# Kernel tuning notes

Hardware: AMD Instinct MI355X
Metric: run time of the kernel (lower is better)

## Reference

```python
import jax, jax.numpy as jnp
import numpy as np

N_SAMPLES = 8192
N_EDGES = 4096
INPUT_DIM = 512
DK = 64
OUTPUT_DIM = 256


def setup_inputs() -> dict:
    key = jax.random.key(0)
    k1, k2, k3, k4, k5, k6 = jax.random.split(key, 6)

    def xavier(k, shape):
        bound = np.sqrt(6.0 / (shape[0] + shape[1])).astype(np.float32)
        return jax.random.uniform(k, shape, jnp.float32, -bound, bound)

    X = jax.random.normal(k1, (N_SAMPLES, INPUT_DIM), jnp.float32)
    Y = jax.random.normal(k2, (N_EDGES, INPUT_DIM), jnp.float32)
    H = jax.random.randint(k3, (N_SAMPLES, N_EDGES), 0, 2, jnp.int32)
    W_q = xavier(k4, (INPUT_DIM, DK))
    W_k = xavier(k5, (INPUT_DIM, DK))
    W_v = xavier(k6, (INPUT_DIM, OUTPUT_DIM))
    return {"X": X, "Y": Y, "H": H, "W_q": W_q, "W_k": W_k, "W_v": W_v}


def reference(X, Y, H, W_q, W_k, W_v):
    # Q: (n_edges, dk), K: (n_samples, dk)
    Q = Y @ W_q
    K = X @ W_k
    scale = jnp.sqrt(jnp.asarray(K.shape[1], jnp.float32))
    # scores: (n_edges, n_samples), masked by hypergraph incidence H.T
    scores = (Q @ K.T) / scale
    scores = jnp.where(H.T == 0, -jnp.inf, scores)
    attn = jax.nn.softmax(scores, axis=-1)
    # attention-weighted vertex features projected by W_v
    return attn @ (X @ W_v)
```

## Files before the change

kernel.cpp:

```cpp
#include <hip/hip_runtime.h>
#include <hip/hip_bf16.h>

#define NS 8192
#define NE 4096
#define DIN 512
#define DK 64
#define DV 256
#define NCHUNK 8
#define CHUNK (NS / NCHUNK)
#define NTILE (CHUNK / 64)

typedef __attribute__((ext_vector_type(8))) short bf16x8;
typedef __attribute__((ext_vector_type(4))) float f32x4;
typedef __attribute__((ext_vector_type(8))) unsigned short ushort8;
typedef __attribute__((ext_vector_type(4))) unsigned short ushort4v;

#define L2E 1.44269504088896f

__device__ __forceinline__ unsigned short f2bf(float f) {
    union { float f; unsigned int u; } v; v.f = f;
    unsigned int u = v.u;
    unsigned int r = u + 0x7fffu + ((u >> 16) & 1u);
    return (unsigned short)(r >> 16);
}

union ProjSmem {
    struct { unsigned short As[64][40]; unsigned short Bst[64][40]; } s;
    unsigned short Ct[64][72];
};

__global__ __launch_bounds__(256, 4) void proj_kernel(
    const float* __restrict__ X, const float* __restrict__ Y,
    const float* __restrict__ Wq, const float* __restrict__ Wk,
    const float* __restrict__ Wv, const int* __restrict__ H,
    unsigned short* __restrict__ Qb, unsigned short* __restrict__ Kb,
    unsigned short* __restrict__ Vt, unsigned int* __restrict__ Hb) {

    int b = blockIdx.x;
    int tid = threadIdx.x;

    if (b >= 704) {
        int pb = b - 704;
        int sg = pb >> 4;
        int e  = (pb & 15) * 256 + tid;
        unsigned word = 0;
        #pragma unroll
        for (int k = 0; k < 32; ++k)
            word |= (unsigned)(H[(size_t)(sg * 32 + k) * NE + e] & 1) << k;
        Hb[(size_t)sg * NE + e] = word;
        return;
    }

    const float* A; const float* B; unsigned short* out;
    int N, m0, n0; float scale; bool tr;
    if (b < 64)       { A = Y; B = Wq; out = Qb; N = 64;  m0 = b * 64;        n0 = 0;            scale = 0.125f * L2E; tr = false; }
    else if (b < 192) { A = X; B = Wk; out = Kb; N = 64;  m0 = (b - 64) * 64; n0 = 0;            scale = 1.0f;         tr = false; }
    else              { int bb = b - 192;
                        A = X; B = Wv; out = Vt; N = 256; m0 = (bb >> 2) * 64; n0 = (bb & 3) * 64; scale = 1.0f;       tr = true; }

    __shared__ ProjSmem sm;
    int lane = tid & 63, w = tid >> 6;
    int c = lane & 15, g = lane >> 4;
    int wr = w >> 1, wc = w & 1;

    f32x4 acc[2][2] = {};

    for (int kt = 0; kt < 16; ++kt) {
        int k0 = kt * 32;
        __syncthreads();
        #pragma unroll
        for (int it = 0; it < 2; ++it) {
            int idx = it * 256 + tid;
            {
                int r = idx >> 3, c4 = (idx & 7) * 4;
                float4 v = *(const float4*)&A[(size_t)(m0 + r) * DIN + k0 + c4];
                ushort4v t; t.x = f2bf(v.x); t.y = f2bf(v.y); t.z = f2bf(v.z); t.w = f2bf(v.w);
                *(ushort4v*)&sm.s.As[r][c4] = t;
            }
            {
                int kk = idx >> 4, c4 = (idx & 15) * 4;
                float4 v = *(const float4*)&B[(size_t)(k0 + kk) * N + n0 + c4];
                sm.s.Bst[c4 + 0][kk] = f2bf(v.x);
                sm.s.Bst[c4 + 1][kk] = f2bf(v.y);
                sm.s.Bst[c4 + 2][kk] = f2bf(v.z);
                sm.s.Bst[c4 + 3][kk] = f2bf(v.w);
            }
        }
        __syncthreads();

        bf16x8 af[2], bfr[2];
        #pragma unroll
        for (int fr = 0; fr < 2; ++fr)
            af[fr] = *(const bf16x8*)&sm.s.As[wr * 32 + fr * 16 + c][8 * g];
        #pragma unroll
        for (int fc = 0; fc < 2; ++fc)
            bfr[fc] = *(const bf16x8*)&sm.s.Bst[wc * 32 + fc * 16 + c][8 * g];
        #pragma unroll
        for (int fr = 0; fr < 2; ++fr)
            #pragma unroll
            for (int fc = 0; fc < 2; ++fc)
                acc[fr][fc] = __builtin_amdgcn_mfma_f32_16x16x32_bf16(af[fr], bfr[fc], acc[fr][fc], 0, 0, 0);
    }

    if (!tr) {
        #pragma unroll
        for (int fr = 0; fr < 2; ++fr)
            #pragma unroll
            for (int fc = 0; fc < 2; ++fc)
                #pragma unroll
                for (int i = 0; i < 4; ++i) {
                    int row = wr * 32 + fr * 16 + 4 * g + i;
                    int col = wc * 32 + fc * 16 + c;
                    out[(size_t)(m0 + row) * N + n0 + col] = f2bf(acc[fr][fc][i] * scale);
                }
    } else {
        __syncthreads();
        #pragma unroll
        for (int fr = 0; fr < 2; ++fr)
            #pragma unroll
            for (int fc = 0; fc < 2; ++fc)
                #pragma unroll
                for (int i = 0; i < 4; ++i) {
                    int row = wr * 32 + fr * 16 + 4 * g + i;
                    int col = wc * 32 + fc * 16 + c;
                    sm.Ct[col][row] = f2bf(acc[fr][fc][i]);
                }
        __syncthreads();
        int nl = tid >> 2, q = tid & 3;
        #pragma unroll
        for (int gg = 0; gg < 2; ++gg) {
            int G = q * 2 + gg;
            int ks = G >> 2, gq = G & 3;
            union { ushort4v h[2]; ushort8 v8; } u;
            u.h[0] = *(const ushort4v*)&sm.Ct[nl][ks * 32 + gq * 4];
            u.h[1] = *(const ushort4v*)&sm.Ct[nl][ks * 32 + 16 + gq * 4];
            *(ushort8*)&out[(size_t)(n0 + nl) * NS + m0 + G * 8] = u.v8;
        }
    }
}

__global__ __launch_bounds__(256, 2) void flash_kernel(
    const unsigned short* __restrict__ Qb, const unsigned short* __restrict__ Kb,
    const unsigned short* __restrict__ Vt, const unsigned int* __restrict__ Hb,
    unsigned int* __restrict__ pacc, float* __restrict__ pm, float* __restrict__ pl) {

    int bid = blockIdx.x;
    int ch = bid & 7, eb = bid >> 3;
    int e0 = eb * 64;
    int sbeg = ch * CHUNK;

    __shared__ unsigned short smem[20480];

    int tid = threadIdx.x, lane = tid & 63, w = tid >> 6;
    int c = lane & 15, g = lane >> 4;
    int eW = e0 + w * 16 + c;
    int cc = tid & 7;
    int swz = (c & 7) << 3;

    bf16x8 qf[2];
    #pragma unroll
    for (int ks = 0; ks < 2; ++ks)
        qf[ks] = *(const bf16x8*)&Qb[(size_t)eW * DK + ks * 32 + 8 * g];

    const unsigned short* baseK[2];
    const unsigned short* baseV[2];
    #pragma unroll
    for (int ks = 0; ks < 2; ++ks) {
        baseK[ks] = &smem[(c * 64 + ks * 32 + 8 * g) ^ swz];
        baseV[ks] = &smem[4096 + ((c * 64 + ks * 32 + 8 * g) ^ swz)];
    }

    int r0 = tid >> 3;
    int cs = cc ^ (r0 & 7);
    const unsigned short* gK[2];
    const unsigned short* gV[8];
    #pragma unroll
    for (int it = 0; it < 2; ++it)
        gK[it] = &Kb[(size_t)(sbeg + it * 32 + r0) * DK + cs * 8];
    #pragma unroll
    for (int it = 0; it < 8; ++it)
        gV[it] = &Vt[(size_t)(it * 32 + r0) * NS + sbeg + cs * 8];

    const unsigned int* hb0 = &Hb[(size_t)(sbeg >> 5) * NE + eW];
    const unsigned int* hb1 = hb0 + NE;

    f32x4 o[16] = {};
    float m = -1e30f, l = 0.0f;

    #pragma unroll 1
    for (int t = 0; t < NTILE; ++t) {
        __syncthreads();

        unsigned hw0 = *hb0; unsigned hw1 = *hb1;
        hb0 += 2 * NE; hb1 += 2 * NE;

        #pragma unroll
        for (int it = 0; it < 2; ++it) {
            __builtin_amdgcn_global_load_lds(
                (const void*)gK[it],
                (void*)((char*)smem + (it * 256 + w * 64) * 16), 16, 0, 0);
            gK[it] += 64 * DK;
        }
        #pragma unroll
        for (int it = 0; it < 8; ++it) {
            __builtin_amdgcn_global_load_lds(
                (const void*)gV[it],
                (void*)((char*)smem + 8192 + (it * 256 + w * 64) * 16), 16, 0, 0);
            gV[it] += 64;
        }

        __syncthreads();

        __builtin_amdgcn_s_setprio(1);
        f32x4 st[4] = {};
        #pragma unroll
        for (int ks = 0; ks < 2; ++ks)
            #pragma unroll
            for (int fr = 0; fr < 4; ++fr) {
                bf16x8 a = *(const bf16x8*)&baseK[ks][fr * 1024];
                st[fr] = __builtin_amdgcn_mfma_f32_16x16x32_bf16(a, qf[ks], st[fr], 0, 0, 0);
            }
        __builtin_amdgcn_s_setprio(0);

        unsigned hs[2] = { hw0 >> (4 * g), hw1 >> (4 * g) };
        float pmax = -1e30f;
        #pragma unroll
        for (int fr = 0; fr < 4; ++fr) {
            unsigned hsf = hs[fr >> 1] >> ((fr & 1) * 16);
            #pragma unroll
            for (int i = 0; i < 4; ++i) {
                float sv = ((hsf >> i) & 1u) ? st[fr][i] : -1e30f;
                st[fr][i] = sv;
                pmax = fmaxf(pmax, sv);
            }
        }
        pmax = fmaxf(pmax, __shfl_xor(pmax, 16));
        pmax = fmaxf(pmax, __shfl_xor(pmax, 32));

        if (!__all(pmax <= m + 8.0f)) {
            float mn = fmaxf(m, pmax);
            float al = exp2f(m - mn);
            l *= al;
            #pragma unroll
            for (int vb = 0; vb < 16; ++vb) o[vb] *= al;
            m = mn;
        }

        float lp = 0.0f;
        #pragma unroll
        for (int fr = 0; fr < 4; ++fr)
            #pragma unroll
            for (int i = 0; i < 4; ++i) {
                float e = exp2f(st[fr][i] - m);
                st[fr][i] = e;
                lp += e;
            }
        lp += __shfl_xor(lp, 16);
        lp += __shfl_xor(lp, 32);
        l += lp;

        unsigned int pk[8];
        #pragma unroll
        for (int fr = 0; fr < 4; ++fr)
            #pragma unroll
            for (int hf = 0; hf < 2; ++hf) {
                union { __hip_bfloat162 h; unsigned int u; } cv;
                cv.h = __float22bfloat162_rn(make_float2(st[fr][2 * hf], st[fr][2 * hf + 1]));
                pk[fr * 2 + hf] = cv.u;
            }

        __builtin_amdgcn_s_setprio(1);
        #pragma unroll
        for (int ks = 0; ks < 2; ++ks) {
            union { unsigned int u[4]; bf16x8 s; } bb;
            bb.u[0] = pk[4 * ks]; bb.u[1] = pk[4 * ks + 1];
            bb.u[2] = pk[4 * ks + 2]; bb.u[3] = pk[4 * ks + 3];
            #pragma unroll
            for (int vb = 0; vb < 16; ++vb) {
                bf16x8 av = *(const bf16x8*)&baseV[ks][vb * 1024];
                o[vb] = __builtin_amdgcn_mfma_f32_16x16x32_bf16(av, bb.s, o[vb], 0, 0, 0);
            }
        }
        __builtin_amdgcn_s_setprio(0);
    }

    size_t base = (size_t)ch * (DV / 2) * NE;
    #pragma unroll
    for (int vb = 0; vb < 16; ++vb)
        #pragma unroll
        for (int ip = 0; ip < 2; ++ip) {
            union { __hip_bfloat162 h; unsigned int u; } cv;
            cv.h = __float22bfloat162_rn(make_float2(o[vb][2 * ip], o[vb][2 * ip + 1]));
            pacc[base + (size_t)(vb * 8 + 2 * g + ip) * NE + eW] = cv.u;
        }
    if (g == 0) {
        pm[ch * NE + eW] = m;
        pl[ch * NE + eW] = l;
    }
}

__global__ __launch_bounds__(256, 4) void combine_kernel(
    const unsigned int* __restrict__ pacc, const float* __restrict__ pm,
    const float* __restrict__ pl, float* __restrict__ out) {

    __shared__ float T[64][68];
    int bid = blockIdx.x;
    int eb = bid & 63, vb = bid >> 6;
    int e0 = eb * 64, v0 = vb * 64;
    int tid = threadIdx.x;
    int el = tid & 63, vh = tid >> 6;
    int e = e0 + el;

    float mv[NCHUNK]; float M = -1e30f;
    #pragma unroll
    for (int chn = 0; chn < NCHUNK; ++chn) {
        mv[chn] = pm[chn * NE + e];
        M = fmaxf(M, mv[chn]);
    }
    float den = 0.0f; float wch[NCHUNK];
    #pragma unroll
    for (int chn = 0; chn < NCHUNK; ++chn) {
        wch[chn] = exp2f(mv[chn] - M);
        den += wch[chn] * pl[chn * NE + e];
    }
    float rden = 1.0f / den;

    #pragma unroll
    for (int kp = 0; kp < 8; ++kp) {
        int vp = vb * 32 + vh * 8 + kp;
        float n0 = 0.0f, n1 = 0.0f;
        #pragma unroll
        for (int chn = 0; chn < NCHUNK; ++chn) {
            unsigned int pk = pacc[((size_t)chn * (DV / 2) + vp) * NE + e];
            n0 += wch[chn] * __uint_as_float(pk << 16);
            n1 += wch[chn] * __uint_as_float(pk & 0xffff0000u);
        }
        T[el][(vh * 8 + kp) * 2]     = n0 * rden;
        T[el][(vh * 8 + kp) * 2 + 1] = n1 * rden;
    }
    __syncthreads();

    int er = tid >> 2, c16 = (tid & 3) * 16;
    #pragma unroll
    for (int j = 0; j < 4; ++j) {
        float4 vv = *(const float4*)&T[er][c16 + 4 * j];
        *(float4*)&out[(size_t)(e0 + er) * DV + v0 + c16 + 4 * j] = vv;
    }
}

#define QB_OFF   ((size_t)0)
#define KB_OFF   (QB_OFF + (size_t)NE * DK * 2)
#define VT_OFF   (KB_OFF + (size_t)NS * DK * 2)
#define PACC_OFF (VT_OFF + (size_t)DV * NS * 2)
#define PM_OFF   (PACC_OFF + (size_t)NCHUNK * (DV / 2) * NE * 4)
#define PL_OFF   (PM_OFF + (size_t)NCHUNK * NE * 4)
#define HB_OFF   (PL_OFF + (size_t)NCHUNK * NE * 4)

extern "C" void kernel_launch(void* const* d_in, const int* in_sizes, int n_in,
                              void* d_out, int out_size, void* d_ws, size_t ws_size,
                              hipStream_t stream) {
    const float* X  = (const float*)d_in[0];
    const float* Y  = (const float*)d_in[1];
    const int*   H  = (const int*)d_in[2];
    const float* Wq = (const float*)d_in[3];
    const float* Wk = (const float*)d_in[4];
    const float* Wv = (const float*)d_in[5];

    char* ws = (char*)d_ws;
    unsigned short* Qb = (unsigned short*)(ws + QB_OFF);
    unsigned short* Kb = (unsigned short*)(ws + KB_OFF);
    unsigned short* Vt = (unsigned short*)(ws + VT_OFF);
    unsigned int* pacc = (unsigned int*)(ws + PACC_OFF);
    float* pm   = (float*)(ws + PM_OFF);
    float* pl   = (float*)(ws + PL_OFF);
    unsigned int* Hb = (unsigned int*)(ws + HB_OFF);

    proj_kernel<<<4800, 256, 0, stream>>>(X, Y, Wq, Wk, Wv, H, Qb, Kb, Vt, Hb);
    flash_kernel<<<512, 256, 0, stream>>>(Qb, Kb, Vt, Hb, pacc, pm, pl);
    combine_kernel<<<256, 256, 0, stream>>>(pacc, pm, pl, (float*)d_out);
}
```

Measured before the change: 92.70 us.

## Stream raw int32 mask tiles into LDS inside flash kernel, drop bit-packing pass

Removes the separate pass in the projection kernel that packed the int32 incidence matrix into bitmasks. The flash kernel now pulls 64x64 int32 mask tiles straight from global memory into LDS with async global_load_lds, alongside the K/V tiles, and reads each mask value from LDS. This saves one full read of H plus the bitmask write and read. In exchange the flash kernel moves 4x more mask bytes per tile through its loads, needs more LDS (which may lower occupancy), and adds LDS reads in the masking step.

```diff
diff --git a/kernel.cpp b/kernel.cpp
--- a/kernel.cpp
+++ b/kernel.cpp
@@ -32,24 +32,12 @@
 __global__ __launch_bounds__(256, 4) void proj_kernel(
     const float* __restrict__ X, const float* __restrict__ Y,
     const float* __restrict__ Wq, const float* __restrict__ Wk,
-    const float* __restrict__ Wv, const int* __restrict__ H,
+    const float* __restrict__ Wv,
     unsigned short* __restrict__ Qb, unsigned short* __restrict__ Kb,
-    unsigned short* __restrict__ Vt, unsigned int* __restrict__ Hb) {
+    unsigned short* __restrict__ Vt) {
 
     int b = blockIdx.x;
     int tid = threadIdx.x;
-
-    if (b >= 704) {
-        int pb = b - 704;
-        int sg = pb >> 4;
-        int e  = (pb & 15) * 256 + tid;
-        unsigned word = 0;
-        #pragma unroll
-        for (int k = 0; k < 32; ++k)
-            word |= (unsigned)(H[(size_t)(sg * 32 + k) * NE + e] & 1) << k;
-        Hb[(size_t)sg * NE + e] = word;
-        return;
-    }
 
     const float* A; const float* B; unsigned short* out;
     int N, m0, n0; float scale; bool tr;
@@ -141,7 +129,7 @@
 
 __global__ __launch_bounds__(256, 2) void flash_kernel(
     const unsigned short* __restrict__ Qb, const unsigned short* __restrict__ Kb,
-    const unsigned short* __restrict__ Vt, const unsigned int* __restrict__ Hb,
+    const unsigned short* __restrict__ Vt, const int* __restrict__ H,
     unsigned int* __restrict__ pacc, float* __restrict__ pm, float* __restrict__ pl) {
 
     int bid = blockIdx.x;
@@ -149,7 +137,7 @@
     int e0 = eb * 64;
     int sbeg = ch * CHUNK;
 
-    __shared__ unsigned short smem[20480];
+    __shared__ unsigned short smem[28672];
 
     int tid = threadIdx.x, lane = tid & 63, w = tid >> 6;
     int c = lane & 15, g = lane >> 4;
@@ -169,20 +157,22 @@
         baseK[ks] = &smem[(c * 64 + ks * 32 + 8 * g) ^ swz];
         baseV[ks] = &smem[4096 + ((c * 64 + ks * 32 + 8 * g) ^ swz)];
     }
+    const int* hL = (const int*)((const char*)smem + 40960) + g * 256 + w * 16 + c;
 
     int r0 = tid >> 3;
     int cs = cc ^ (r0 & 7);
     const unsigned short* gK[2];
     const unsigned short* gV[8];
+    const int* gH[4];
     #pragma unroll
     for (int it = 0; it < 2; ++it)
         gK[it] = &Kb[(size_t)(sbeg + it * 32 + r0) * DK + cs * 8];
     #pragma unroll
     for (int it = 0; it < 8; ++it)
         gV[it] = &Vt[(size_t)(it * 32 + r0) * NS + sbeg + cs * 8];
-
-    const unsigned int* hb0 = &Hb[(size_t)(sbeg >> 5) * NE + eW];
-    const unsigned int* hb1 = hb0 + NE;
+    #pragma unroll
+    for (int it = 0; it < 4; ++it)
+        gH[it] = &H[(size_t)(sbeg + it * 16 + (tid >> 4)) * NE + e0 + (tid & 15) * 4];
 
     f32x4 o[16] = {};
     float m = -1e30f, l = 0.0f;
@@ -190,9 +180,6 @@
     #pragma unroll 1
     for (int t = 0; t < NTILE; ++t) {
         __syncthreads();
-
-        unsigned hw0 = *hb0; unsigned hw1 = *hb1;
-        hb0 += 2 * NE; hb1 += 2 * NE;
 
         #pragma unroll
         for (int it = 0; it < 2; ++it) {
@@ -208,6 +195,13 @@
                 (void*)((char*)smem + 8192 + (it * 256 + w * 64) * 16), 16, 0, 0);
             gV[it] += 64;
         }
+        #pragma unroll
+        for (int it = 0; it < 4; ++it) {
+            __builtin_amdgcn_global_load_lds(
+                (const void*)gH[it],
+                (void*)((char*)smem + 40960 + (it * 256 + w * 64) * 16), 16, 0, 0);
+            gH[it] += 64 * NE;
+        }
 
         __syncthreads();
 
@@ -222,18 +216,16 @@
             }
         __builtin_amdgcn_s_setprio(0);
 
-        unsigned hs[2] = { hw0 >> (4 * g), hw1 >> (4 * g) };
         float pmax = -1e30f;
         #pragma unroll
-        for (int fr = 0; fr < 4; ++fr) {
-            unsigned hsf = hs[fr >> 1] >> ((fr & 1) * 16);
+        for (int fr = 0; fr < 4; ++fr)
             #pragma unroll
             for (int i = 0; i < 4; ++i) {
-                float sv = ((hsf >> i) & 1u) ? st[fr][i] : -1e30f;
+                int hv = hL[fr * 1024 + i * 64];
+                float sv = hv ? st[fr][i] : -1e30f;
                 st[fr][i] = sv;
                 pmax = fmaxf(pmax, sv);
             }
-        }
         pmax = fmaxf(pmax, __shfl_xor(pmax, 16));
         pmax = fmaxf(pmax, __shfl_xor(pmax, 32));
 
@@ -354,7 +346,6 @@
 #define PACC_OFF (VT_OFF + (size_t)DV * NS * 2)
 #define PM_OFF   (PACC_OFF + (size_t)NCHUNK * (DV / 2) * NE * 4)
 #define PL_OFF   (PM_OFF + (size_t)NCHUNK * NE * 4)
-#define HB_OFF   (PL_OFF + (size_t)NCHUNK * NE * 4)
 
 extern "C" void kernel_launch(void* const* d_in, const int* in_sizes, int n_in,
                               void* d_out, int out_size, void* d_ws, size_t ws_size,
@@ -373,9 +364,8 @@
     unsigned int* pacc = (unsigned int*)(ws + PACC_OFF);
     float* pm   = (float*)(ws + PM_OFF);
     float* pl   = (float*)(ws + PL_OFF);
-    unsigned int* Hb = (unsigned int*)(ws + HB_OFF);
-
-    proj_kernel<<<4800, 256, 0, stream>>>(X, Y, Wq, Wk, Wv, H, Qb, Kb, Vt, Hb);
-    flash_kernel<<<512, 256, 0, stream>>>(Qb, Kb, Vt, Hb, pacc, pm, pl);
+
+    proj_kernel<<<704, 256, 0, stream>>>(X, Y, Wq, Wk, Wv, Qb, Kb, Vt);
+    flash_kernel<<<512, 256, 0, stream>>>(Qb, Kb, Vt, H, pacc, pm, pl);
     combine_kernel<<<256, 256, 0, stream>>>(pacc, pm, pl, (float*)d_out);
 }
```

Result: faster. 83.28 us (-10.2%).
